# Optimization experiments

Hardware: AMD Instinct MI355X
Metric: run time of the kernel (lower is better)

## Reference

```python
import jax, jax.numpy as jnp
import numpy as np

EPS = 1e-5

@jax.custom_vjp
def binarize(x):
    return jnp.sign(x)

def _bin_fwd(x):
    return jnp.sign(x), None

def _bin_bwd(_, g):
    return (g,)  # straight-through estimator (matches .data overwrite trick)

binarize.defvjp(_bin_fwd, _bin_bwd)

def conv2d(x, w, b):
    y = jax.lax.conv_general_dilated(x, w, (1, 1), 'VALID',
                                     dimension_numbers=('NCHW', 'OIHW', 'NCHW'))
    return y + b[None, :, None, None]

def bn2d(x, g, be, m, v):
    inv = g / jnp.sqrt(v + EPS)
    return (x - m[None, :, None, None]) * inv[None, :, None, None] + be[None, :, None, None]

def bn1d(x, m, v):  # affine=False, eval mode
    return (x - m) / jnp.sqrt(v + EPS)

def maxpool2(x):
    return jax.lax.reduce_window(x, -jnp.inf, jax.lax.max, (1, 1, 2, 2), (1, 1, 2, 2), 'VALID')

def hardtanh(x):
    return jnp.clip(x, -1.0, 1.0)

def setup_inputs() -> dict:
    key = jax.random.key(0)
    ks = jax.random.split(key, 16)
    B = 8192
    d = {
        'x': jax.random.normal(ks[0], (B, 3, 32, 32), jnp.float32),
        'w1': jax.random.normal(ks[1], (16, 3, 5, 5), jnp.float32),
        'b1': jax.random.normal(ks[2], (16,), jnp.float32) * 0.1,
        'g1': jnp.ones((16,), jnp.float32), 'be1': jnp.zeros((16,), jnp.float32),
        'm1': jnp.zeros((16,), jnp.float32), 'v1': jnp.ones((16,), jnp.float32),
        'w2': jax.random.normal(ks[3], (32, 16, 5, 5), jnp.float32),
        'b2': jax.random.normal(ks[4], (32,), jnp.float32) * 0.1,
        'g2': jnp.ones((32,), jnp.float32), 'be2': jnp.zeros((32,), jnp.float32),
        'm2': jnp.zeros((32,), jnp.float32), 'v2': jnp.ones((32,), jnp.float32),
        'w3': jax.random.normal(ks[5], (64, 32, 5, 5), jnp.float32),
        'b3': jax.random.normal(ks[6], (64,), jnp.float32) * 0.1,
        'g3': jnp.ones((64,), jnp.float32), 'be3': jnp.zeros((64,), jnp.float32),
        'm3': jnp.zeros((64,), jnp.float32), 'v3': jnp.ones((64,), jnp.float32),
        'fw1': jax.random.normal(ks[7], (128, 64), jnp.float32),
        'fb1': jax.random.normal(ks[8], (128,), jnp.float32) * 0.1,
        'cm1': jnp.zeros((128,), jnp.float32), 'cv1': jnp.ones((128,), jnp.float32),
        'fw2': jax.random.normal(ks[9], (128, 128), jnp.float32),
        'fb2': jax.random.normal(ks[10], (128,), jnp.float32) * 0.1,
        'cm2': jnp.zeros((128,), jnp.float32), 'cv2': jnp.ones((128,), jnp.float32),
        'fw3': jax.random.normal(ks[11], (10, 128), jnp.float32),
        'cm3': jnp.zeros((10,), jnp.float32), 'cv3': jnp.ones((10,), jnp.float32),
    }
    return d

def reference(x, w1, b1, g1, be1, m1, v1, w2, b2, g2, be2, m2, v2,
              w3, b3, g3, be3, m3, v3, fw1, fb1, cm1, cv1,
              fw2, fb2, cm2, cv2, fw3, cm3, cv3):
    # features: conv1 input has 3 channels -> NOT binarized (first-layer rule)
    h = conv2d(x, binarize(w1), b1)
    h = maxpool2(hardtanh(bn2d(h, g1, be1, m1, v1)))
    h = conv2d(binarize(h), binarize(w2), b2)
    h = maxpool2(hardtanh(bn2d(h, g2, be2, m2, v2)))
    h = conv2d(binarize(h), binarize(w3), b3)
    h = hardtanh(bn2d(h, g3, be3, m3, v3))
    h = h.reshape(-1, 64)  # spatial is 1x1 by construction
    # classifier (all linear inputs binarized: in_features != 784)
    h = binarize(h) @ binarize(fw1).T + fb1
    h = bn1d(h, cm1, cv1)
    h = binarize(h) @ binarize(fw2).T + fb2
    h = bn1d(h, cm2, cv2)
    h = binarize(h) @ binarize(fw3).T
    h = bn1d(h, cm3, cv3)
    return jax.nn.log_softmax(h, axis=-1)
```

## Files before the change

kernel.cpp:

```cpp
#include <hip/hip_runtime.h>
#include <cstdint>

#define EPS 1e-5f

#define A1_OFF   0ull
#define W2M_OFF  4030464ull
#define W3M_OFF  4033664ull
#define FW1M_OFF 4040064ull
#define FW2M_OFF 4041088ull
#define FW3M_OFF 4043136ull
#define T1_OFF   4043296ull
#define T2_OFF   4043360ull
#define T3_OFF   4043488ull
#define TC1_OFF  4043744ull
#define TC2_OFF  4044256ull
#define BF_OFF   4044768ull
#define FIXCNT_OFF 4061184ull
#define FIXREC_OFF 4061248ull
#define FIXCAP   32768u

using bf16x8 = __attribute__((ext_vector_type(8))) short;
using f32x4  = __attribute__((ext_vector_type(4))) float;

union FragU { unsigned int u[4]; bf16x8 f; };

__device__ inline unsigned short rne_bf16(float f) {
    unsigned int u = __float_as_uint(f);
    return (unsigned short)((u + 0x7FFFu + ((u >> 16) & 1u)) >> 16);
}

__global__ void setup_kernel(
    const float* __restrict__ w1, const float* __restrict__ w2,
    const float* __restrict__ w3,
    const float* __restrict__ fw1, const float* __restrict__ fw2,
    const float* __restrict__ fw3,
    const float* __restrict__ b1, const float* __restrict__ g1,
    const float* __restrict__ be1, const float* __restrict__ m1,
    const float* __restrict__ v1,
    const float* __restrict__ b2, const float* __restrict__ g2,
    const float* __restrict__ be2, const float* __restrict__ m2,
    const float* __restrict__ v2,
    const float* __restrict__ b3, const float* __restrict__ g3,
    const float* __restrict__ be3, const float* __restrict__ m3,
    const float* __restrict__ v3,
    const float* __restrict__ fb1, const float* __restrict__ cm1,
    const float* __restrict__ fb2, const float* __restrict__ cm2,
    unsigned int* __restrict__ w2m, unsigned int* __restrict__ w3m,
    unsigned long long* __restrict__ fw1m, unsigned long long* __restrict__ fw2m,
    unsigned long long* __restrict__ fw3m,
    float* __restrict__ t1, float* __restrict__ t2, float* __restrict__ t3,
    float* __restrict__ tc1, float* __restrict__ tc2,
    uint4* __restrict__ bfrag, unsigned int* __restrict__ fixcnt)
{
    const int tid = threadIdx.x;
    const int blk = blockIdx.x;

    if (blk == 0) {
        if (tid < 16) t1[tid] = m1[tid] - be1[tid]*sqrtf(v1[tid]+EPS)/g1[tid] - b1[tid];
        if (tid < 32) t2[tid] = m2[tid] - be2[tid]*sqrtf(v2[tid]+EPS)/g2[tid] - b2[tid];
        if (tid < 64) t3[tid] = m3[tid] - be3[tid]*sqrtf(v3[tid]+EPS)/g3[tid] - b3[tid];
        if (tid < 128) { tc1[tid] = cm1[tid] - fb1[tid]; tc2[tid] = cm2[tid] - fb2[tid]; }
        for (int t = tid; t < 32*25; t += 256) {
            int oc = t / 25, pos = t % 25;
            unsigned int mk = 0;
            for (int ic = 0; ic < 16; ++ic)
                if (w2[(oc*16 + ic)*25 + pos] > 0.0f) mk |= 1u << ic;
            w2m[t] = mk;
        }
    } else if (blk == 1) {
        for (int t = tid; t < 64*25; t += 256) {
            int oc = t / 25, pos = t % 25;
            unsigned int mk = 0;
            for (int ic = 0; ic < 32; ++ic)
                if (w3[(oc*32 + ic)*25 + pos] > 0.0f) mk |= 1u << ic;
            w3m[t] = mk;
        }
    } else if (blk == 2) {
        for (int t = tid; t < 128; t += 256) {
            unsigned long long mk = 0;
            for (int i = 0; i < 64; ++i)
                if (fw1[t*64 + i] > 0.0f) mk |= 1ull << i;
            fw1m[t] = mk;
        }
    } else if (blk == 3) {
        for (int t = tid; t < 128; t += 256) {
            unsigned long long lo = 0, hi = 0;
            for (int i = 0; i < 64; ++i) {
                if (fw2[t*128 + i]      > 0.0f) lo |= 1ull << i;
                if (fw2[t*128 + 64 + i] > 0.0f) hi |= 1ull << i;
            }
            fw2m[2*t] = lo; fw2m[2*t+1] = hi;
        }
        if (tid < 10) {
            unsigned long long lo = 0, hi = 0;
            for (int i = 0; i < 64; ++i) {
                if (fw3[tid*128 + i]      > 0.0f) lo |= 1ull << i;
                if (fw3[tid*128 + 64 + i] > 0.0f) hi |= 1ull << i;
            }
            fw3m[2*tid] = lo; fw3m[2*tid+1] = hi;
        }
    } else {
        if (tid == 0) fixcnt[0] = 0;
        if (tid < 64) {
            const int oc = tid & 15, q = tid >> 4;
            for (int d = 0; d < 4; ++d)
                for (int kg = 0; kg < 4; ++kg) {
                    int ck = kg*4 + q;
                    unsigned short s[8];
                    for (int j = 0; j < 8; ++j) {
                        int kx = j - d;
                        unsigned short v = 0;
                        if (ck < 15 && kx >= 0 && kx < 5)
                            v = (w1[oc*75 + ck*5 + kx] > 0.0f) ? 0x3F80 : 0xBF80;
                        s[j] = v;
                    }
                    uint4 o;
                    o.x = (unsigned int)s[0] | ((unsigned int)s[1] << 16);
                    o.y = (unsigned int)s[2] | ((unsigned int)s[3] << 16);
                    o.z = (unsigned int)s[4] | ((unsigned int)s[5] << 16);
                    o.w = (unsigned int)s[6] | ((unsigned int)s[7] << 16);
                    bfrag[(d*4 + kg)*64 + tid] = o;
                }
        }
    }
}

__global__ __launch_bounds__(128) void convpool1_kernel(
    const float* __restrict__ x, const float* __restrict__ t1,
    const uint4* __restrict__ bfrag, unsigned int* __restrict__ a1u,
    unsigned int* __restrict__ fixcnt, uint2* __restrict__ fixrec)
{
    __shared__ alignas(16) unsigned short xh[3*36*44];
    __shared__ alignas(16) unsigned short xl[3*36*44];
    __shared__ unsigned short pk16[196];

    const int tid  = threadIdx.x;
    const int lane = tid & 63;
    const int wv   = tid >> 6;
    const int quad = lane >> 4;
    const int me   = lane & 15;
    const int n0   = blockIdx.x * 4;

    FragU B[16];
    #pragma unroll
    for (int i = 0; i < 16; ++i)
        *(uint4*)B[i].u = bfrag[i*64 + lane];

    int basekg[4];
    #pragma unroll
    for (int kg = 0; kg < 4; ++kg) {
        int ck = kg*4 + quad;
        int ckc = ck < 15 ? ck : 14;
        int c = ckc / 5, ky = ckc % 5;
        basekg[kg] = (c*36 + ky + me)*44;
    }
    int se[6];
    #pragma unroll
    for (int k = 0; k < 6; ++k) {
        int j = tid + k*128;
        int c = j >> 8, f = j & 255, row = f >> 3, q = f & 7;
        se[k] = (c*36 + row)*44 + 4*q;
    }

    const float thr = t1[me];
    #pragma unroll 1
    for (int i = 0; i < 4; ++i) {
        if (i > 0 && tid < 98)
            a1u[(size_t)(n0 + i - 1)*98 + tid] =
                (unsigned int)pk16[2*tid] | ((unsigned int)pk16[2*tid + 1] << 16);
        {
            const float4* xg = (const float4*)(x + (size_t)(n0 + i) * 3072);
            float4 v[6];
            #pragma unroll
            for (int k = 0; k < 6; ++k) v[k] = xg[tid + k*128];
            #pragma unroll
            for (int k = 0; k < 6; ++k) {
                unsigned short h0 = rne_bf16(v[k].x), h1 = rne_bf16(v[k].y),
                               h2 = rne_bf16(v[k].z), h3 = rne_bf16(v[k].w);
                float r0 = v[k].x - __uint_as_float((unsigned int)h0 << 16);
                float r1 = v[k].y - __uint_as_float((unsigned int)h1 << 16);
                float r2 = v[k].z - __uint_as_float((unsigned int)h2 << 16);
                float r3 = v[k].w - __uint_as_float((unsigned int)h3 << 16);
                uint2 ph, pl;
                ph.x = (unsigned int)h0 | ((unsigned int)h1 << 16);
                ph.y = (unsigned int)h2 | ((unsigned int)h3 << 16);
                pl.x = (unsigned int)rne_bf16(r0) | ((unsigned int)rne_bf16(r1) << 16);
                pl.y = (unsigned int)rne_bf16(r2) | ((unsigned int)rne_bf16(r3) << 16);
                *(uint2*)&xh[se[k]] = ph;
                *(uint2*)&xl[se[k]] = pl;
            }
        }
        __syncthreads();

        const int n = n0 + i;
        #pragma unroll 1
        for (int ti = 0; ti < 7; ++ti) {
            const int task = wv*7 + ti;
            const int g = task >> 1, tt = task & 1;
            const int off = 4*g + tt*704;

            f32x4 acc[4];
            #pragma unroll
            for (int d = 0; d < 4; ++d) acc[d] = (f32x4){0.f, 0.f, 0.f, 0.f};

            #pragma unroll
            for (int kg = 0; kg < 4; ++kg) {
                int idx = basekg[kg] + off;
                FragU ah, al;
                uint2 p0 = *(const uint2*)&xh[idx];
                uint2 p1 = *(const uint2*)&xh[idx + 4];
                ah.u[0] = p0.x; ah.u[1] = p0.y; ah.u[2] = p1.x; ah.u[3] = p1.y;
                uint2 q0 = *(const uint2*)&xl[idx];
                uint2 q1 = *(const uint2*)&xl[idx + 4];
                al.u[0] = q0.x; al.u[1] = q0.y; al.u[2] = q1.x; al.u[3] = q1.y;
                #pragma unroll
                for (int d = 0; d < 4; ++d)
                    acc[d] = __builtin_amdgcn_mfma_f32_16x16x32_bf16(
                        ah.f, B[d*4 + kg].f, acc[d], 0, 0, 0);
                #pragma unroll
                for (int d = 0; d < 4; ++d)
                    acc[d] = __builtin_amdgcn_mfma_f32_16x16x32_bf16(
                        al.f, B[d*4 + kg].f, acc[d], 0, 0, 0);
            }

            const int valid = !(tt == 1 && quad == 3);
            #pragma unroll
            for (int dp = 0; dp < 2; ++dp) {
                f32x4 A0 = acc[2*dp], A1 = acc[2*dp + 1];
                #pragma unroll
                for (int r = 0; r < 2; ++r) {
                    float h = fmaxf(fmaxf(A0[2*r], A0[2*r+1]),
                                    fmaxf(A1[2*r], A1[2*r+1]));
                    int bit = h > thr;
                    if (valid && fabsf(h - thr) < 2e-3f) {
                        int cell = (tt*8 + quad*2 + r)*14 + 2*g + dp;
                        unsigned int slot = atomicAdd(fixcnt, 1u);
                        if (slot < FIXCAP) {
                            uint2 rec;
                            rec.x = (unsigned int)n;
                            rec.y = ((unsigned int)cell << 8) | (unsigned int)me;
                            fixrec[slot] = rec;
                        }
                    }
                    unsigned long long mk = __ballot(bit);
                    if (me == 0 && valid)
                        pk16[(tt*8 + quad*2 + r)*14 + 2*g + dp] =
                            (unsigned short)(mk >> (quad*16));
                }
            }
        }
        __syncthreads();
    }
    if (tid < 98)
        a1u[(size_t)(n0 + 3)*98 + tid] =
            (unsigned int)pk16[2*tid] | ((unsigned int)pk16[2*tid + 1] << 16);
}

__global__ void fixup_kernel(
    const float* __restrict__ x, const float* __restrict__ w1,
    const float* __restrict__ t1,
    const unsigned int* __restrict__ fixcnt, const uint2* __restrict__ fixrec,
    unsigned int* __restrict__ a1u)
{
    unsigned int cnt = fixcnt[0];
    if (cnt > FIXCAP) cnt = FIXCAP;
    for (unsigned int i = blockIdx.x*blockDim.x + threadIdx.x; i < cnt;
         i += gridDim.x*blockDim.x) {
        uint2 rec = fixrec[i];
        int n = (int)rec.x;
        int cell = (int)(rec.y >> 8);
        int oc = (int)(rec.y & 255u);
        int py = cell / 14, px = cell % 14;
        float thr = t1[oc];
        double best = -1e300;
        #pragma unroll 1
        for (int d2 = 0; d2 < 4; ++d2) {
            int oy = 2*py + (d2 >> 1), ox = 2*px + (d2 & 1);
            double s = 0.0;
            #pragma unroll 1
            for (int c2 = 0; c2 < 3; ++c2)
                #pragma unroll 1
                for (int ky2 = 0; ky2 < 5; ++ky2)
                    #pragma unroll 1
                    for (int kx2 = 0; kx2 < 5; ++kx2) {
                        float wv = w1[oc*75 + c2*25 + ky2*5 + kx2];
                        float xv = x[(size_t)n*3072 + c2*1024 + (oy + ky2)*32 + ox + kx2];
                        s += (wv > 0.0f) ? (double)xv : -(double)xv;
                    }
            best = fmax(best, s);
        }
        unsigned int mask = 1u << ((cell & 1)*16 + oc);
        unsigned int* wp = &a1u[(size_t)n*98 + (cell >> 1)];
        if (best > (double)thr) atomicOr(wp, mask);
        else                    atomicAnd(wp, ~mask);
    }
}

__global__ __launch_bounds__(256) void conv2tail_kernel(
    const unsigned int* __restrict__ a1u, const unsigned int* __restrict__ w2m,
    const float* __restrict__ t2,
    const unsigned int* __restrict__ w3m, const float* __restrict__ t3,
    const unsigned long long* __restrict__ fw1m, const float* __restrict__ tc1,
    const unsigned long long* __restrict__ fw2m, const float* __restrict__ tc2,
    const unsigned long long* __restrict__ fw3m,
    const float* __restrict__ cm3, const float* __restrict__ cv3,
    float* __restrict__ out)
{
    __shared__ unsigned int M[8][14][16];
    __shared__ unsigned int P[8][14][16];
    __shared__ unsigned int Q[8][13][16];
    __shared__ unsigned int a2l[8][25];
    __shared__ unsigned int w3s[1600];
    __shared__ unsigned long long fw1s[128], fw2s[256], fw3s[20];
    __shared__ float t3s[64], tc1s[128], tc2s[128], cm3s[16], cv3s[16];

    const int tid = threadIdx.x;
    const int lane = tid & 63;
    const int wv = tid >> 6;
    const int n0 = blockIdx.x * 8;

    for (int i = tid; i < 1600; i += 256) w3s[i] = w3m[i];
    if (tid < 128) { fw1s[tid] = fw1m[tid]; tc1s[tid] = tc1[tid]; tc2s[tid] = tc2[tid]; }
    fw2s[tid] = fw2m[tid];
    if (tid < 20) fw3s[tid] = fw3m[tid];
    if (tid < 64) t3s[tid] = t3[tid];
    if (tid < 10) { cm3s[tid] = cm3[tid]; cv3s[tid] = cv3[tid]; }

    for (int i = tid; i < 8*98; i += 256) {
        unsigned int v = a1u[(size_t)n0*98 + i];
        int e = 2*i;
        int im = e / 196, r = e - im*196;
        int y0 = r / 14, c0 = r - y0*14;
        int r1 = r + 1, y1 = r1 / 14, c1 = r1 - y1*14;
        M[im][y0][c0] = v & 0xffffu;
        M[im][y1][c1] = v >> 16;
    }
    __syncthreads();
    for (int i = tid; i < 8*14*13; i += 256) {
        int im = i / 182, r = i - im*182, y = r / 13, j = r - y*13;
        P[im][y][j] = M[im][y][j] | (M[im][y][j+1] << 16);
    }
    for (int i = tid; i < 8*13*14; i += 256) {
        int im = i / 182, r = i - im*182, y = r / 14, j = r - y*14;
        Q[im][y][j] = M[im][y][j] | (M[im][y+1][j] << 16);
    }
    __syncthreads();

    const int img = tid >> 5, oc = tid & 31;
    unsigned int wrow[25];
    #pragma unroll
    for (int k = 0; k < 25; ++k) wrow[k] = w2m[oc*25 + k];
    unsigned int wp[5][2], wc0, wc1, wcs;
    #pragma unroll
    for (int ky = 0; ky < 5; ++ky) {
        wp[ky][0] = wrow[ky*5]     | (wrow[ky*5+1] << 16);
        wp[ky][1] = wrow[ky*5 + 2] | (wrow[ky*5+3] << 16);
    }
    wc0 = wrow[4]  | (wrow[9]  << 16);
    wc1 = wrow[14] | (wrow[19] << 16);
    wcs = wrow[24];
    const float thr = t2[oc];

    unsigned int bits = 0;
    int hprev[5];
    #pragma unroll 2
    for (int oy = 0; oy < 10; ++oy) {
        unsigned int Pr[5][12];
        #pragma unroll
        for (int ky = 0; ky < 5; ++ky) {
            const uint4* pr = (const uint4*)&P[img][oy + ky][0];
            uint4 a = pr[0], b = pr[1], c = pr[2];
            Pr[ky][0]=a.x; Pr[ky][1]=a.y; Pr[ky][2]=a.z; Pr[ky][3]=a.w;
            Pr[ky][4]=b.x; Pr[ky][5]=b.y; Pr[ky][6]=b.z; Pr[ky][7]=b.w;
            Pr[ky][8]=c.x; Pr[ky][9]=c.y; Pr[ky][10]=c.z; Pr[ky][11]=c.w;
        }
        unsigned int Qa[10], Qb[10], Ms[10];
        {
            const uint4* qa = (const uint4*)&Q[img][oy][4];
            const uint2* qa2 = (const uint2*)&Q[img][oy][12];
            uint4 a = qa[0], b = qa[1]; uint2 c = qa2[0];
            Qa[0]=a.x; Qa[1]=a.y; Qa[2]=a.z; Qa[3]=a.w;
            Qa[4]=b.x; Qa[5]=b.y; Qa[6]=b.z; Qa[7]=b.w; Qa[8]=c.x; Qa[9]=c.y;
            const uint4* qb = (const uint4*)&Q[img][oy+2][4];
            const uint2* qb2 = (const uint2*)&Q[img][oy+2][12];
            uint4 d = qb[0], e = qb[1]; uint2 f = qb2[0];
            Qb[0]=d.x; Qb[1]=d.y; Qb[2]=d.z; Qb[3]=d.w;
            Qb[4]=e.x; Qb[5]=e.y; Qb[6]=e.z; Qb[7]=e.w; Qb[8]=f.x; Qb[9]=f.y;
            const uint4* ms = (const uint4*)&M[img][oy+4][4];
            const uint2* ms2 = (const uint2*)&M[img][oy+4][12];
            uint4 g = ms[0], h = ms[1]; uint2 k2 = ms2[0];
            Ms[0]=g.x; Ms[1]=g.y; Ms[2]=g.z; Ms[3]=g.w;
            Ms[4]=h.x; Ms[5]=h.y; Ms[6]=h.z; Ms[7]=h.w; Ms[8]=k2.x; Ms[9]=k2.y;
        }
        int X[10];
        #pragma unroll
        for (int ox = 0; ox < 10; ++ox) {
            int s = 0;
            #pragma unroll
            for (int ky = 0; ky < 5; ++ky)
                s += __popc(Pr[ky][ox] ^ wp[ky][0]) + __popc(Pr[ky][ox+2] ^ wp[ky][1]);
            s += __popc(Qa[ox] ^ wc0) + __popc(Qb[ox] ^ wc1) + __popc(Ms[ox] ^ wcs);
            X[ox] = s;
        }
        #pragma unroll
        for (int px = 0; px < 5; ++px) {
            int h = min(X[2*px], X[2*px+1]);
            if ((oy & 1) == 0) hprev[px] = h;
            else {
                int mn = min(hprev[px], h);
                if ((float)(400 - 2*mn) > thr) bits |= 1u << ((oy >> 1)*5 + px);
            }
        }
    }
    #pragma unroll
    for (int cell = 0; cell < 25; ++cell) {
        unsigned long long m = __ballot((bits >> cell) & 1);
        if (lane == 0)  a2l[2*wv][cell]     = (unsigned int)m;
        if (lane == 32) a2l[2*wv + 1][cell] = (unsigned int)(m >> 32);
    }
    __syncthreads();

    #pragma unroll 1
    for (int rnd = 0; rnd < 2; ++rnd) {
        const int im = wv + 4*rnd;
        const int n = n0 + im;

        unsigned int av[25];
        #pragma unroll
        for (int k = 0; k < 25; ++k) av[k] = a2l[im][k];

        int X = 0;
        #pragma unroll
        for (int k = 0; k < 25; ++k) X += __popc(av[k] ^ w3s[lane*25 + k]);
        float d3 = (float)(800 - 2*X);
        unsigned long long a3 = __ballot(d3 > t3s[lane]);

        int o1 = lane + 64;
        int d0 = 64 - 2*(int)__popcll(a3 ^ fw1s[lane]);
        int d1 = 64 - 2*(int)__popcll(a3 ^ fw1s[o1]);
        unsigned long long a4lo = __ballot((float)d0 > tc1s[lane]);
        unsigned long long a4hi = __ballot((float)d1 > tc1s[o1]);

        int e0 = 128 - 2*(int)(__popcll(a4lo ^ fw2s[2*lane]) + __popcll(a4hi ^ fw2s[2*lane+1]));
        int e1 = 128 - 2*(int)(__popcll(a4lo ^ fw2s[2*o1])   + __popcll(a4hi ^ fw2s[2*o1+1]));
        unsigned long long a5lo = __ballot((float)e0 > tc2s[lane]);
        unsigned long long a5hi = __ballot((float)e1 > tc2s[o1]);

        float y = -1e30f;
        if (lane < 10) {
            int f = 128 - 2*(int)(__popcll(a5lo ^ fw3s[2*lane]) + __popcll(a5hi ^ fw3s[2*lane+1]));
            y = ((float)f - cm3s[lane]) / sqrtf(cv3s[lane] + EPS);
        }
        float mx = y;
        #pragma unroll
        for (int off = 8; off > 0; off >>= 1) mx = fmaxf(mx, __shfl_xor(mx, off, 16));
        float s = (lane < 10) ? expf(y - mx) : 0.0f;
        #pragma unroll
        for (int off = 8; off > 0; off >>= 1) s += __shfl_xor(s, off, 16);
        if (lane < 10) out[(size_t)n*10 + lane] = y - mx - logf(s);
    }
}

extern "C" void kernel_launch(void* const* d_in, const int* in_sizes, int n_in,
                              void* d_out, int out_size, void* d_ws, size_t ws_size,
                              hipStream_t stream)
{
    const float* x   = (const float*)d_in[0];
    const float* w1  = (const float*)d_in[1];
    const float* b1  = (const float*)d_in[2];
    const float* g1  = (const float*)d_in[3];
    const float* be1 = (const float*)d_in[4];
    const float* m1  = (const float*)d_in[5];
    const float* v1  = (const float*)d_in[6];
    const float* w2  = (const float*)d_in[7];
    const float* b2  = (const float*)d_in[8];
    const float* g2  = (const float*)d_in[9];
    const float* be2 = (const float*)d_in[10];
    const float* m2  = (const float*)d_in[11];
    const float* v2  = (const float*)d_in[12];
    const float* w3  = (const float*)d_in[13];
    const float* b3  = (const float*)d_in[14];
    const float* g3  = (const float*)d_in[15];
    const float* be3 = (const float*)d_in[16];
    const float* m3  = (const float*)d_in[17];
    const float* v3  = (const float*)d_in[18];
    const float* fw1 = (const float*)d_in[19];
    const float* fb1 = (const float*)d_in[20];
    const float* cm1 = (const float*)d_in[21];
    const float* fw2 = (const float*)d_in[23];
    const float* fb2 = (const float*)d_in[24];
    const float* cm2 = (const float*)d_in[25];
    const float* fw3 = (const float*)d_in[27];
    const float* cm3 = (const float*)d_in[28];
    const float* cv3 = (const float*)d_in[29];

    char* ws = (char*)d_ws;
    unsigned int*       a1u  = (unsigned int*)(ws + A1_OFF);
    unsigned int*       w2m  = (unsigned int*)(ws + W2M_OFF);
    unsigned int*       w3m  = (unsigned int*)(ws + W3M_OFF);
    unsigned long long* fw1m = (unsigned long long*)(ws + FW1M_OFF);
    unsigned long long* fw2m = (unsigned long long*)(ws + FW2M_OFF);
    unsigned long long* fw3m = (unsigned long long*)(ws + FW3M_OFF);
    float* t1  = (float*)(ws + T1_OFF);
    float* t2  = (float*)(ws + T2_OFF);
    float* t3  = (float*)(ws + T3_OFF);
    float* tc1 = (float*)(ws + TC1_OFF);
    float* tc2 = (float*)(ws + TC2_OFF);
    uint4* bfrag = (uint4*)(ws + BF_OFF);
    unsigned int* fixcnt = (unsigned int*)(ws + FIXCNT_OFF);
    uint2* fixrec = (uint2*)(ws + FIXREC_OFF);

    setup_kernel<<<5, 256, 0, stream>>>(
        w1, w2, w3, fw1, fw2, fw3,
        b1, g1, be1, m1, v1,
        b2, g2, be2, m2, v2,
        b3, g3, be3, m3, v3,
        fb1, cm1, fb2, cm2,
        w2m, w3m, fw1m, fw2m, fw3m, t1, t2, t3, tc1, tc2, bfrag, fixcnt);

    convpool1_kernel<<<2048, 128, 0, stream>>>(x, t1, bfrag, a1u, fixcnt, fixrec);
    fixup_kernel<<<64, 256, 0, stream>>>(x, w1, t1, fixcnt, fixrec, a1u);
    conv2tail_kernel<<<1024, 256, 0, stream>>>(a1u, w2m, t2, w3m, t3,
                                               fw1m, tc1, fw2m, tc2, fw3m,
                                               cm3, cv3, (float*)d_out);
}
```

Measured before the change: 329.3 us.

## Prefetch next image into registers during conv1 MFMA compute

The conv1 kernel now loads the next image's input from global memory into registers before the current image's MFMA loop, then converts and stores it to shared memory after the compute. The goal is to hide global load latency behind compute. It also swaps the round-to-nearest conversion of the bf16 residual for plain truncation, which is cheaper but less accurate. The weight-mask prep for fw2/fw3 is spread across more threads. The cost is more registers held during the compute loop, which may lower occupancy.

```diff
diff --git a/kernel.cpp b/kernel.cpp
--- a/kernel.cpp
+++ b/kernel.cpp
@@ -83,21 +83,19 @@
             fw1m[t] = mk;
         }
     } else if (blk == 3) {
-        for (int t = tid; t < 128; t += 256) {
-            unsigned long long lo = 0, hi = 0;
-            for (int i = 0; i < 64; ++i) {
-                if (fw2[t*128 + i]      > 0.0f) lo |= 1ull << i;
-                if (fw2[t*128 + 64 + i] > 0.0f) hi |= 1ull << i;
-            }
-            fw2m[2*t] = lo; fw2m[2*t+1] = hi;
-        }
-        if (tid < 10) {
-            unsigned long long lo = 0, hi = 0;
-            for (int i = 0; i < 64; ++i) {
-                if (fw3[tid*128 + i]      > 0.0f) lo |= 1ull << i;
-                if (fw3[tid*128 + 64 + i] > 0.0f) hi |= 1ull << i;
-            }
-            fw3m[2*tid] = lo; fw3m[2*tid+1] = hi;
+        {
+            int row = tid >> 1, half = tid & 1;
+            unsigned long long mk = 0;
+            for (int i = 0; i < 64; ++i)
+                if (fw2[row*128 + half*64 + i] > 0.0f) mk |= 1ull << i;
+            fw2m[2*row + half] = mk;
+        }
+        if (tid < 20) {
+            int row = tid >> 1, half = tid & 1;
+            unsigned long long mk = 0;
+            for (int i = 0; i < 64; ++i)
+                if (fw3[row*128 + half*64 + i] > 0.0f) mk |= 1ull << i;
+            fw3m[tid] = mk;
         }
     } else {
         if (tid == 0) fixcnt[0] = 0;
@@ -163,34 +161,38 @@
     }
 
     const float thr = t1[me];
+
+    {
+        const float4* xg = (const float4*)(x + (size_t)n0 * 3072);
+        #pragma unroll
+        for (int k = 0; k < 6; ++k) {
+            float4 v = xg[tid + k*128];
+            unsigned short h0 = rne_bf16(v.x), h1 = rne_bf16(v.y),
+                           h2 = rne_bf16(v.z), h3 = rne_bf16(v.w);
+            float r0 = v.x - __uint_as_float((unsigned int)h0 << 16);
+            float r1 = v.y - __uint_as_float((unsigned int)h1 << 16);
+            float r2 = v.z - __uint_as_float((unsigned int)h2 << 16);
+            float r3 = v.w - __uint_as_float((unsigned int)h3 << 16);
+            uint2 ph, pl;
+            ph.x = (unsigned int)h0 | ((unsigned int)h1 << 16);
+            ph.y = (unsigned int)h2 | ((unsigned int)h3 << 16);
+            pl.x = (__float_as_uint(r0) >> 16) | (__float_as_uint(r1) & 0xffff0000u);
+            pl.y = (__float_as_uint(r2) >> 16) | (__float_as_uint(r3) & 0xffff0000u);
+            *(uint2*)&xh[se[k]] = ph;
+            *(uint2*)&xl[se[k]] = pl;
+        }
+    }
+    __syncthreads();
+
     #pragma unroll 1
     for (int i = 0; i < 4; ++i) {
-        if (i > 0 && tid < 98)
-            a1u[(size_t)(n0 + i - 1)*98 + tid] =
-                (unsigned int)pk16[2*tid] | ((unsigned int)pk16[2*tid + 1] << 16);
-        {
-            const float4* xg = (const float4*)(x + (size_t)(n0 + i) * 3072);
-            float4 v[6];
+        float4 pf[6];
+        const int more = (i < 3);
+        if (more) {
+            const float4* xg = (const float4*)(x + (size_t)(n0 + i + 1) * 3072);
             #pragma unroll
-            for (int k = 0; k < 6; ++k) v[k] = xg[tid + k*128];
-            #pragma unroll
-            for (int k = 0; k < 6; ++k) {
-                unsigned short h0 = rne_bf16(v[k].x), h1 = rne_bf16(v[k].y),
-                               h2 = rne_bf16(v[k].z), h3 = rne_bf16(v[k].w);
-                float r0 = v[k].x - __uint_as_float((unsigned int)h0 << 16);
-                float r1 = v[k].y - __uint_as_float((unsigned int)h1 << 16);
-                float r2 = v[k].z - __uint_as_float((unsigned int)h2 << 16);
-                float r3 = v[k].w - __uint_as_float((unsigned int)h3 << 16);
-                uint2 ph, pl;
-                ph.x = (unsigned int)h0 | ((unsigned int)h1 << 16);
-                ph.y = (unsigned int)h2 | ((unsigned int)h3 << 16);
-                pl.x = (unsigned int)rne_bf16(r0) | ((unsigned int)rne_bf16(r1) << 16);
-                pl.y = (unsigned int)rne_bf16(r2) | ((unsigned int)rne_bf16(r3) << 16);
-                *(uint2*)&xh[se[k]] = ph;
-                *(uint2*)&xl[se[k]] = pl;
-            }
-        }
-        __syncthreads();
+            for (int k = 0; k < 6; ++k) pf[k] = xg[tid + k*128];
+        }
 
         const int n = n0 + i;
         #pragma unroll 1
@@ -250,10 +252,31 @@
             }
         }
         __syncthreads();
-    }
-    if (tid < 98)
-        a1u[(size_t)(n0 + 3)*98 + tid] =
-            (unsigned int)pk16[2*tid] | ((unsigned int)pk16[2*tid + 1] << 16);
+
+        if (tid < 98)
+            a1u[(size_t)n*98 + tid] =
+                (unsigned int)pk16[2*tid] | ((unsigned int)pk16[2*tid + 1] << 16);
+        if (more) {
+            #pragma unroll
+            for (int k = 0; k < 6; ++k) {
+                float4 v = pf[k];
+                unsigned short h0 = rne_bf16(v.x), h1 = rne_bf16(v.y),
+                               h2 = rne_bf16(v.z), h3 = rne_bf16(v.w);
+                float r0 = v.x - __uint_as_float((unsigned int)h0 << 16);
+                float r1 = v.y - __uint_as_float((unsigned int)h1 << 16);
+                float r2 = v.z - __uint_as_float((unsigned int)h2 << 16);
+                float r3 = v.w - __uint_as_float((unsigned int)h3 << 16);
+                uint2 ph, pl;
+                ph.x = (unsigned int)h0 | ((unsigned int)h1 << 16);
+                ph.y = (unsigned int)h2 | ((unsigned int)h3 << 16);
+                pl.x = (__float_as_uint(r0) >> 16) | (__float_as_uint(r1) & 0xffff0000u);
+                pl.y = (__float_as_uint(r2) >> 16) | (__float_as_uint(r3) & 0xffff0000u);
+                *(uint2*)&xh[se[k]] = ph;
+                *(uint2*)&xl[se[k]] = pl;
+            }
+        }
+        __syncthreads();
+    }
 }
 
 __global__ void fixup_kernel(
```

After: 334.2 us. About the same (+1.5%).
